# Kernel tuning notes

Hardware: AMD Instinct MI355X
Metric: run time of the kernel (lower is better)

## Reference

```python
import jax, jax.numpy as jnp
import numpy as np

DIM = 1024
HEADS = 16


def setup_inputs() -> dict:
    key = jax.random.key(0)
    ks = jax.random.split(key, 8)
    b, n, d = 2, 2048, DIM
    x = jax.random.normal(ks[0], (b, n, d), dtype=jnp.float32)
    # Linear(dim, 3*dim, bias=False): weight stored as [dim, 3*dim] (pre-transposed)
    W_qkv = jax.random.normal(ks[1], (d, 3 * d), dtype=jnp.float32) * (d ** -0.5)
    # Linear(dim, dim) with bias
    W_out = jax.random.normal(ks[2], (d, d), dtype=jnp.float32) * (d ** -0.5)
    b_out = jnp.zeros((d,), dtype=jnp.float32)
    alpha = jnp.ones((1,), dtype=jnp.float32)
    beta = jnp.zeros((1,), dtype=jnp.float32) + 0.5  # nonzero so softmax path is exercised
    gamma = jnp.zeros((1,), dtype=jnp.float32) + 0.1
    return {"x": x, "W_qkv": W_qkv, "W_out": W_out, "b_out": b_out,
            "alpha": alpha, "beta": beta, "gamma": gamma}


def reference(x, W_qkv, W_out, b_out, alpha, beta, gamma):
    b, n, d = x.shape
    h = HEADS
    hd = d // h
    scale = d ** -0.5  # note: full dim, as in the original module
    qkv = x @ W_qkv  # [b, n, 3d]
    q, k, v = jnp.split(qkv, 3, axis=-1)
    # [b, n, d] -> [b, h, n, hd]
    to_heads = lambda t: t.reshape(b, n, h, hd).transpose(0, 2, 1, 3)
    q, k, v = to_heads(q), to_heads(k), to_heads(v)
    dots = jnp.einsum("bhqd,bhkd->bhqk", q, k) * scale  # [b, h, n, n]
    attn = (alpha[0] * jnp.eye(n, dtype=x.dtype)
            + beta[0] * jax.nn.softmax(dots, axis=-1)
            - gamma[0] / n)
    out = jnp.einsum("bhqk,bhkd->bhqd", attn, v)  # [b, h, n, hd]
    out = out.transpose(0, 2, 1, 3).reshape(b, n, d)
    return out @ W_out + b_out
```

## Files before the change

### kernel.cpp

```cpp
#include <hip/hip_runtime.h>
#include <hip/hip_bf16.h>

#define DEVI __device__ __forceinline__

typedef __attribute__((ext_vector_type(8))) short bf16x8;
typedef __attribute__((ext_vector_type(4))) short bf16x4;
typedef __attribute__((ext_vector_type(4))) float f32x4;

DEVI unsigned short f2bf(float f) {
    unsigned u = __float_as_uint(f);
    u += 0x7FFF + ((u >> 16) & 1);
    return (unsigned short)(u >> 16);
}
DEVI float bf2f(unsigned short h) {
    return __uint_as_float(((unsigned)h) << 16);
}
DEVI f32x4 mfma16(bf16x8 a, bf16x8 b, f32x4 c) {
    return __builtin_amdgcn_mfma_f32_16x16x32_bf16(a, b, c, 0, 0, 0);
}
DEVI void gload_lds16(const void* g, void* l) {
    __builtin_amdgcn_global_load_lds(
        (const __attribute__((address_space(1))) unsigned int*)g,
        (__attribute__((address_space(3))) unsigned int*)l, 16, 0, 0);
}

DEVI void wt_body(const float* __restrict__ W, unsigned short* __restrict__ Wt,
                  int N, int n0, int k0, float sc, int tid,
                  unsigned short (*T)[72])
{
#pragma unroll
    for (int j = 0; j < 4; ++j) {
        int idx = tid + j * 256;
        int kk = idx >> 4, c4 = (idx & 15) << 2;
        float4 v = *(const float4*)(W + (size_t)(k0 + kk) * N + n0 + c4);
        T[c4 + 0][kk] = f2bf(v.x * sc); T[c4 + 1][kk] = f2bf(v.y * sc);
        T[c4 + 2][kk] = f2bf(v.z * sc); T[c4 + 3][kk] = f2bf(v.w * sc);
    }
    __syncthreads();
#pragma unroll
    for (int j = 0; j < 4; ++j) {
        int idx = tid + j * 256;
        int n = idx >> 4, c4 = (idx & 15) << 2;
        *(bf16x4*)(Wt + (size_t)(n0 + n) * 1024 + k0 + c4) = *(bf16x4*)&T[n][c4];
    }
}

__global__ __launch_bounds__(256) void k_prep(
    const float* __restrict__ X, const float* __restrict__ Wqkv,
    const float* __restrict__ Wout,
    unsigned short* __restrict__ Xb, unsigned short* __restrict__ Wt1,
    unsigned short* __restrict__ Wt2)
{
    __shared__ unsigned short T[64][72];
    const int tid = threadIdx.x;
    const int bid = blockIdx.x;
    const float QSC = 1.4426950408889634f / 32.0f;
    if (bid < 1024) {
        int i = bid * 256 + tid;
#pragma unroll
        for (int j = 0; j < 4; ++j) {
            int idx = i + j * 262144;
            float4 v = *(const float4*)(X + (size_t)idx * 4);
            bf16x4 hv;
            hv[0] = (short)f2bf(v.x); hv[1] = (short)f2bf(v.y);
            hv[2] = (short)f2bf(v.z); hv[3] = (short)f2bf(v.w);
            *(bf16x4*)(Xb + (size_t)idx * 4) = hv;
        }
    } else if (bid < 1792) {
        int idx = bid - 1024;
        int n0 = (idx % 48) * 64, k0 = (idx / 48) * 64;
        wt_body(Wqkv, Wt1, 3072, n0, k0, (n0 < 1024) ? QSC : 1.0f, tid, T);
    } else {
        int idx = bid - 1792;
        int n0 = (idx & 15) * 64, k0 = (idx >> 4) * 64;
        wt_body(Wout, Wt2, 1024, n0, k0, 1.0f, tid, T);
    }
}

__global__ __launch_bounds__(256) void k_gemm1(
    const unsigned short* __restrict__ A, const unsigned short* __restrict__ B,
    unsigned short* __restrict__ C)
{
    __shared__ unsigned short Sh[18432];
    unsigned short* As = Sh;
    unsigned short* Bs = Sh + 8192;
    const int tid = threadIdx.x, lane = tid & 63, wid = tid >> 6;
    const int wr = (wid >> 1) * 64, wc = (wid & 1) * 64;
    const int row0 = blockIdx.y * 128, col0 = blockIdx.x * 128;
    const int rsel = lane & 15, kgr = (lane >> 4) * 8;
    const int lr = lane >> 3, lc = (lane & 7) * 8;

    f32x4 acc[4][4];
#pragma unroll
    for (int i = 0; i < 4; ++i)
#pragma unroll
        for (int j = 0; j < 4; ++j) acc[i][j] = (f32x4){0.f, 0.f, 0.f, 0.f};

    for (int k0 = 0; k0 < 1024; k0 += 64) {
        __syncthreads();
#pragma unroll
        for (int i = 0; i < 4; ++i) {
            int rb = wid * 32 + i * 8;
            gload_lds16(A + (size_t)(row0 + rb + lr) * 1024 + k0 + lc, As + rb * 64);
            gload_lds16(B + (size_t)(col0 + rb + lr) * 1024 + k0 + lc, Bs + rb * 64);
        }
        __syncthreads();
#pragma unroll
        for (int ks = 0; ks < 2; ++ks) {
            bf16x8 a[4], b[4];
            int ko = ks * 32 + kgr;
#pragma unroll
            for (int mi = 0; mi < 4; ++mi)
                a[mi] = *(const bf16x8*)(As + (wr + mi * 16 + rsel) * 64 + ko);
#pragma unroll
            for (int nj = 0; nj < 4; ++nj)
                b[nj] = *(const bf16x8*)(Bs + (wc + nj * 16 + rsel) * 64 + ko);
#pragma unroll
            for (int mi = 0; mi < 4; ++mi)
#pragma unroll
                for (int nj = 0; nj < 4; ++nj)
                    acc[mi][nj] = mfma16(a[mi], b[nj], acc[mi][nj]);
        }
    }
    __syncthreads();
    unsigned short (*wb)[72] = (unsigned short (*)[72])(Sh + wid * 4608);
    const int g4 = (lane >> 4) << 2;
#pragma unroll
    for (int mi = 0; mi < 4; ++mi)
#pragma unroll
        for (int nj = 0; nj < 4; ++nj)
#pragma unroll
            for (int r = 0; r < 4; ++r)
                wb[mi * 16 + g4 + r][nj * 16 + rsel] = f2bf(acc[mi][nj][r]);
#pragma unroll
    for (int rr = 0; rr < 8; ++rr) {
        int row = rr * 8 + (lane >> 3);
        int c8 = (lane & 7) * 8;
        bf16x8 v = *(const bf16x8*)&wb[row][c8];
        *(bf16x8*)(C + (size_t)(row0 + wr + row) * 3072 + col0 + wc + c8) = v;
    }
}

__global__ __launch_bounds__(256) void k_vt(
    const unsigned short* __restrict__ qkv, unsigned short* __restrict__ Vt,
    float* __restrict__ vsum)
{
    __shared__ unsigned short T[64][72];
    __shared__ float ps[64];
    const int tid = threadIdx.x, lane = tid & 63, wid = tid >> 6;
    const int bh = blockIdx.y, b = bh >> 4, h = bh & 15;
    const int n0 = blockIdx.x * 64;
    const unsigned short* src = qkv + (size_t)(b * 2048 + n0) * 3072 + 2048 + h * 64;
#pragma unroll
    for (int j = 0; j < 2; ++j) {
        int idx = tid + j * 256;
        int n = idx >> 3, c8 = (idx & 7) << 3;
        *(bf16x8*)&T[n][c8] = *(const bf16x8*)(src + (size_t)n * 3072 + c8);
    }
    if (tid < 64) ps[tid] = 0.f;
    __syncthreads();
#pragma unroll
    for (int i = 0; i < 16; ++i) {
        int dv = wid * 16 + i;
        Vt[((size_t)bh * 64 + dv) * 2048 + n0 + lane] = T[lane][dv];
    }
    {
        const int col = tid & 63, qtr = tid >> 6;
        float s = 0.f;
#pragma unroll
        for (int i = 0; i < 16; ++i) s += bf2f(T[qtr * 16 + i][col]);
        atomicAdd(&ps[col], s);
        __syncthreads();
        if (tid < 64) atomicAdd(&vsum[bh * 64 + tid], ps[tid]);
    }
}

__global__ __launch_bounds__(256) void k_attn(
    const unsigned short* __restrict__ qkv, const unsigned short* __restrict__ Vt,
    const float* __restrict__ vsum,
    const float* __restrict__ alpha_p, const float* __restrict__ beta_p,
    const float* __restrict__ gamma_p,
    unsigned short* __restrict__ AO)
{
    __shared__ unsigned short Ks[4][64][64];
    __shared__ unsigned short Vs[4][64][64];
    __shared__ unsigned short Ps[4][32][64];
    const int tid = threadIdx.x, lane = tid & 63, wid = tid >> 6;
    const int swz = (blockIdx.x & 7) * 64 + (blockIdx.x >> 3);
    const int bh = swz >> 4, qtb = swz & 15;
    const int b = bh >> 4, h = bh & 15;
    const int q0 = qtb * 128;
    const int rsel = lane & 15, g = lane >> 4;
    const int g4 = g << 2;
    const int wq0 = wid * 32;
    const int r7 = rsel & 7;

    bf16x8 bq[2][2];
#pragma unroll
    for (int qt = 0; qt < 2; ++qt) {
        const unsigned short* qrow =
            qkv + (size_t)(b * 2048 + q0 + wq0 + qt * 16 + rsel) * 3072 + h * 64;
        bq[qt][0] = *(const bf16x8*)(qrow + g * 8);
        bq[qt][1] = *(const bf16x8*)(qrow + 32 + g * 8);
    }

    const int sr = lane >> 3;
    const int ss = (lane & 7) ^ sr;
    const int rb0 = wid * 16, rb1 = wid * 16 + 8;
    const unsigned short* kp0 = qkv + (size_t)(b * 2048) * 3072 + 1024 + h * 64
                              + (size_t)(rb0 + sr) * 3072 + ss * 8;
    const unsigned short* kp1 = kp0 + (size_t)8 * 3072;
    const unsigned short* vp0 = Vt + (size_t)bh * 64 * 2048
                              + (size_t)(rb0 + sr) * 2048 + ss * 8;
    const unsigned short* vp1 = vp0 + (size_t)8 * 2048;
    const size_t KADV = (size_t)64 * 3072;

    f32x4 o[2][4], ol[2];
#pragma unroll
    for (int qt = 0; qt < 2; ++qt) {
#pragma unroll
        for (int dj = 0; dj < 4; ++dj) o[qt][dj] = (f32x4){0.f, 0.f, 0.f, 0.f};
        ol[qt] = (f32x4){0.f, 0.f, 0.f, 0.f};
    }
    bf16x8 ones;
#pragma unroll
    for (int e = 0; e < 8; ++e) ones[e] = (short)0x3F80;

#define STAGE(BUF)                                                             \
    {                                                                          \
        gload_lds16(kp0, &Ks[BUF][rb0][0]);                                    \
        gload_lds16(kp1, &Ks[BUF][rb1][0]);                                    \
        gload_lds16(vp0, &Vs[BUF][rb0][0]);                                    \
        gload_lds16(vp1, &Vs[BUF][rb1][0]);                                    \
        kp0 += KADV; kp1 += KADV; vp0 += 64; vp1 += 64;                        \
    }

    STAGE(0); STAGE(1);
    asm volatile("s_waitcnt vmcnt(0)" ::: "memory");
    __syncthreads();

#define QK(CUR, S)                                                             \
    {                                                                          \
        _Pragma("unroll")                                                      \
        for (int qt = 0; qt < 2; ++qt)                                         \
            _Pragma("unroll")                                                  \
            for (int kj = 0; kj < 4; ++kj)                                     \
                S[qt][kj] = (f32x4){0.f, 0.f, 0.f, 0.f};                       \
        __builtin_amdgcn_s_setprio(1);                                         \
        _Pragma("unroll")                                                      \
        for (int ks = 0; ks < 2; ++ks) {                                       \
            const int sl = ((ks * 4 + g) ^ r7) * 8;                            \
            bf16x8 ak[4];                                                      \
            _Pragma("unroll")                                                  \
            for (int kj = 0; kj < 4; ++kj)                                     \
                ak[kj] = *(const bf16x8*)(&Ks[CUR][kj * 16 + rsel][sl]);       \
            _Pragma("unroll")                                                  \
            for (int qt = 0; qt < 2; ++qt)                                     \
                _Pragma("unroll")                                              \
                for (int kj = 0; kj < 4; ++kj)                                 \
                    S[qt][kj] = mfma16(ak[kj], bq[qt][ks], S[qt][kj]);         \
        }                                                                      \
        __builtin_amdgcn_s_setprio(0);                                         \
    }

#define EPV(CUR, S)                                                            \
    {                                                                          \
        _Pragma("unroll")                                                      \
        for (int qt = 0; qt < 2; ++qt)                                         \
            _Pragma("unroll")                                                  \
            for (int kj = 0; kj < 4; ++kj) {                                   \
                float p0 = __builtin_amdgcn_exp2f(S[qt][kj][0]);               \
                float p1 = __builtin_amdgcn_exp2f(S[qt][kj][1]);               \
                float p2 = __builtin_amdgcn_exp2f(S[qt][kj][2]);               \
                float p3 = __builtin_amdgcn_exp2f(S[qt][kj][3]);               \
                union { __hip_bfloat162 h2[2]; uint2 u; } pk;                  \
                pk.h2[0] = __float22bfloat162_rn(make_float2(p0, p1));         \
                pk.h2[1] = __float22bfloat162_rn(make_float2(p2, p3));         \
                const int slot16 = (kj * 2 + (g >> 1)) ^ r7;                   \
                *(uint2*)(&Ps[wid][qt * 16 + rsel][slot16 * 8 + (g & 1) * 4])  \
                    = pk.u;                                                    \
            }                                                                  \
        __builtin_amdgcn_s_setprio(1);                                         \
        _Pragma("unroll")                                                      \
        for (int ks = 0; ks < 2; ++ks) {                                       \
            const int sl = ((ks * 4 + g) ^ r7) * 8;                            \
            bf16x8 pa0 = *(const bf16x8*)(&Ps[wid][rsel][sl]);                 \
            bf16x8 pa1 = *(const bf16x8*)(&Ps[wid][16 + rsel][sl]);            \
            bf16x8 vb[4];                                                      \
            _Pragma("unroll")                                                  \
            for (int dj = 0; dj < 4; ++dj)                                     \
                vb[dj] = *(const bf16x8*)(&Vs[CUR][dj * 16 + rsel][sl]);       \
            _Pragma("unroll")                                                  \
            for (int dj = 0; dj < 4; ++dj) {                                   \
                o[0][dj] = mfma16(pa0, vb[dj], o[0][dj]);                      \
                o[1][dj] = mfma16(pa1, vb[dj], o[1][dj]);                      \
            }                                                                  \
            ol[0] = mfma16(pa0, ones, ol[0]);                                  \
            ol[1] = mfma16(pa1, ones, ol[1]);                                  \
        }                                                                      \
        __builtin_amdgcn_s_setprio(0);                                         \
    }

#define PAIR(C0, C1, DOPF)                                                     \
    {                                                                          \
        f32x4 s0[2][4], s1[2][4];                                              \
        if (DOPF) { STAGE(C0 ^ 2); STAGE(C1 ^ 2); }                            \
        QK(C0, s0);                                                            \
        QK(C1, s1);                                                            \
        EPV(C0, s0);                                                           \
        EPV(C1, s1);                                                           \
        asm volatile("s_waitcnt vmcnt(0)" ::: "memory");                       \
        __syncthreads();                                                       \
    }

#pragma unroll 1
    for (int i = 0; i < 8; ++i) {
        PAIR(0, 1, true);
        PAIR(2, 3, (i < 7));
    }
#undef PAIR
#undef EPV
#undef QK
#undef STAGE

    const float alpha = *alpha_p, beta = *beta_p;
    const float gn = (*gamma_p) / 2048.0f;
#pragma unroll
    for (int qt = 0; qt < 2; ++qt) {
        float linv[4];
#pragma unroll
        for (int r = 0; r < 4; ++r)
            linv[r] = beta / ol[qt][r];
#pragma unroll
        for (int dj = 0; dj < 4; ++dj)
#pragma unroll
            for (int r = 0; r < 4; ++r) {
                int qrow = q0 + wq0 + qt * 16 + g4 + r;
                int dv = dj * 16 + rsel;
                float ov = o[qt][dj][r] * linv[r];
                float vdiag = bf2f(qkv[(size_t)(b * 2048 + qrow) * 3072 + 2048 + h * 64 + dv]);
                float vs = vsum[bh * 64 + dv];
                float res = ov + alpha * vdiag - gn * vs;
                AO[(size_t)(b * 2048 + qrow) * 1024 + h * 64 + dv] = f2bf(res);
            }
    }
}

__global__ __launch_bounds__(256) void k_gemm2(
    const unsigned short* __restrict__ A, const unsigned short* __restrict__ B,
    const float* __restrict__ bias, float* __restrict__ Out)
{
    __shared__ unsigned short As[64 * 64];
    __shared__ unsigned short Bs[64 * 64];
    const int tid = threadIdx.x, lane = tid & 63, wid = tid >> 6;
    const int wr = (wid >> 1) * 32, wc = (wid & 1) * 32;
    const int row0 = blockIdx.y * 64, col0 = blockIdx.x * 64;
    const int rsel = lane & 15, kgr = (lane >> 4) * 8;
    const int lr = lane >> 3, lc = (lane & 7) * 8;

    f32x4 acc[2][2];
#pragma unroll
    for (int i = 0; i < 2; ++i)
#pragma unroll
        for (int j = 0; j < 2; ++j) acc[i][j] = (f32x4){0.f, 0.f, 0.f, 0.f};

    for (int k0 = 0; k0 < 1024; k0 += 64) {
        __syncthreads();
#pragma unroll
        for (int i = 0; i < 2; ++i) {
            int rb = wid * 16 + i * 8;
            gload_lds16(A + (size_t)(row0 + rb + lr) * 1024 + k0 + lc, As + rb * 64);
            gload_lds16(B + (size_t)(col0 + rb + lr) * 1024 + k0 + lc, Bs + rb * 64);
        }
        __syncthreads();
#pragma unroll
        for (int ks = 0; ks < 2; ++ks) {
            bf16x8 a[2], b[2];
            int ko = ks * 32 + kgr;
#pragma unroll
            for (int mi = 0; mi < 2; ++mi)
                a[mi] = *(const bf16x8*)(As + (wr + mi * 16 + rsel) * 64 + ko);
#pragma unroll
            for (int nj = 0; nj < 2; ++nj)
                b[nj] = *(const bf16x8*)(Bs + (wc + nj * 16 + rsel) * 64 + ko);
#pragma unroll
            for (int mi = 0; mi < 2; ++mi)
#pragma unroll
                for (int nj = 0; nj < 2; ++nj)
                    acc[mi][nj] = mfma16(a[mi], b[nj], acc[mi][nj]);
        }
    }
    const int rbase = row0 + wr + ((lane >> 4) << 2);
    const int cbase = col0 + wc + rsel;
#pragma unroll
    for (int mi = 0; mi < 2; ++mi)
#pragma unroll
        for (int nj = 0; nj < 2; ++nj) {
            int gc = cbase + nj * 16;
            float bv = bias[gc];
#pragma unroll
            for (int r = 0; r < 4; ++r)
                Out[(size_t)(rbase + mi * 16 + r) * 1024 + gc] = acc[mi][nj][r] + bv;
        }
}

extern "C" void kernel_launch(void* const* d_in, const int* in_sizes, int n_in,
                              void* d_out, int out_size, void* d_ws, size_t ws_size,
                              hipStream_t stream) {
    const float* x     = (const float*)d_in[0];
    const float* Wqkv  = (const float*)d_in[1];
    const float* Wout  = (const float*)d_in[2];
    const float* bout  = (const float*)d_in[3];
    const float* alpha = (const float*)d_in[4];
    const float* beta  = (const float*)d_in[5];
    const float* gamma = (const float*)d_in[6];
    float* out = (float*)d_out;

    char* ws = (char*)d_ws;
    unsigned short* Xb  = (unsigned short*)(ws);
    unsigned short* Wt1 = (unsigned short*)(ws + 8388608);
    unsigned short* Wt2 = (unsigned short*)(ws + 14680064);
    unsigned short* qkv = (unsigned short*)(ws + 16777216);
    unsigned short* Vt  = (unsigned short*)(ws + 41943040);
    float* vsum         = (float*)(ws + 50331648);
    unsigned short* AO  = Xb;

    hipMemsetAsync(vsum, 0, 2048 * sizeof(float), stream);
    k_prep<<<2048, 256, 0, stream>>>(x, Wqkv, Wout, Xb, Wt1, Wt2);
    k_gemm1<<<dim3(24, 32), 256, 0, stream>>>(Xb, Wt1, qkv);
    k_vt<<<dim3(32, 32), 256, 0, stream>>>(qkv, Vt, vsum);
    k_attn<<<512, 256, 0, stream>>>(qkv, Vt, vsum, alpha, beta, gamma, AO);
    k_gemm2<<<dim3(16, 64), 256, 0, stream>>>(AO, Wt2, bout, out);
}
```

Measured before the change: 141.2 us.

## Fuse V transpose and column-sum into GEMM1 epilogue, fold memset into prep

Removes the separate k_vt kernel. The QKV GEMM epilogue now writes the transposed V tile from its LDS staging buffer and accumulates per-head V column sums with shuffles and atomics. The vsum memset is moved into block 0 of the prep kernel. This saves two launches and a re-read of V from global memory. In exchange, the V-column GEMM blocks do extra scattered 2-byte stores and more atomics. The sums now come from fp32 accumulators rather than bf16-rounded values.

```diff
diff --git a/kernel.cpp b/kernel.cpp
--- a/kernel.cpp
+++ b/kernel.cpp
@@ -49,13 +49,18 @@
     const float* __restrict__ X, const float* __restrict__ Wqkv,
     const float* __restrict__ Wout,
     unsigned short* __restrict__ Xb, unsigned short* __restrict__ Wt1,
-    unsigned short* __restrict__ Wt2)
+    unsigned short* __restrict__ Wt2, float* __restrict__ vsum)
 {
     __shared__ unsigned short T[64][72];
     const int tid = threadIdx.x;
     const int bid = blockIdx.x;
     const float QSC = 1.4426950408889634f / 32.0f;
     if (bid < 1024) {
+        if (bid == 0) {
+            float4 z = (float4){0.f, 0.f, 0.f, 0.f};
+            ((float4*)vsum)[tid] = z;
+            ((float4*)vsum)[tid + 256] = z;
+        }
         int i = bid * 256 + tid;
 #pragma unroll
         for (int j = 0; j < 4; ++j) {
@@ -79,7 +84,8 @@
 
 __global__ __launch_bounds__(256) void k_gemm1(
     const unsigned short* __restrict__ A, const unsigned short* __restrict__ B,
-    unsigned short* __restrict__ C)
+    unsigned short* __restrict__ C, unsigned short* __restrict__ Vt,
+    float* __restrict__ vsum)
 {
     __shared__ unsigned short Sh[18432];
     unsigned short* As = Sh;
@@ -139,39 +145,26 @@
         bf16x8 v = *(const bf16x8*)&wb[row][c8];
         *(bf16x8*)(C + (size_t)(row0 + wr + row) * 3072 + col0 + wc + c8) = v;
     }
-}
-
-__global__ __launch_bounds__(256) void k_vt(
-    const unsigned short* __restrict__ qkv, unsigned short* __restrict__ Vt,
-    float* __restrict__ vsum)
-{
-    __shared__ unsigned short T[64][72];
-    __shared__ float ps[64];
-    const int tid = threadIdx.x, lane = tid & 63, wid = tid >> 6;
-    const int bh = blockIdx.y, b = bh >> 4, h = bh & 15;
-    const int n0 = blockIdx.x * 64;
-    const unsigned short* src = qkv + (size_t)(b * 2048 + n0) * 3072 + 2048 + h * 64;
-#pragma unroll
-    for (int j = 0; j < 2; ++j) {
-        int idx = tid + j * 256;
-        int n = idx >> 3, c8 = (idx & 7) << 3;
-        *(bf16x8*)&T[n][c8] = *(const bf16x8*)(src + (size_t)n * 3072 + c8);
-    }
-    if (tid < 64) ps[tid] = 0.f;
-    __syncthreads();
-#pragma unroll
-    for (int i = 0; i < 16; ++i) {
-        int dv = wid * 16 + i;
-        Vt[((size_t)bh * 64 + dv) * 2048 + n0 + lane] = T[lane][dv];
-    }
-    {
-        const int col = tid & 63, qtr = tid >> 6;
-        float s = 0.f;
-#pragma unroll
-        for (int i = 0; i < 16; ++i) s += bf2f(T[qtr * 16 + i][col]);
-        atomicAdd(&ps[col], s);
-        __syncthreads();
-        if (tid < 64) atomicAdd(&vsum[bh * 64 + tid], ps[tid]);
+
+    if (col0 >= 2048) {
+        const int b_ = row0 >> 11;
+        const int n0 = (row0 & 2047) + wr;
+        const int bh = b_ * 16 + ((col0 + wc - 2048) >> 6);
+#pragma unroll
+        for (int nj = 0; nj < 4; ++nj) {
+            float s = 0.f;
+#pragma unroll
+            for (int mi = 0; mi < 4; ++mi)
+#pragma unroll
+                for (int r = 0; r < 4; ++r) s += acc[mi][nj][r];
+            s += __shfl_xor(s, 16);
+            s += __shfl_xor(s, 32);
+            if (lane < 16) atomicAdd(&vsum[bh * 64 + nj * 16 + rsel], s);
+        }
+        unsigned short* vtb = Vt + (size_t)bh * 64 * 2048 + n0 + lane;
+#pragma unroll 8
+        for (int dv = 0; dv < 64; ++dv)
+            vtb[(size_t)dv * 2048] = wb[lane][dv];
     }
 }
 
@@ -425,10 +418,8 @@
     float* vsum         = (float*)(ws + 50331648);
     unsigned short* AO  = Xb;
 
-    hipMemsetAsync(vsum, 0, 2048 * sizeof(float), stream);
-    k_prep<<<2048, 256, 0, stream>>>(x, Wqkv, Wout, Xb, Wt1, Wt2);
-    k_gemm1<<<dim3(24, 32), 256, 0, stream>>>(Xb, Wt1, qkv);
-    k_vt<<<dim3(32, 32), 256, 0, stream>>>(qkv, Vt, vsum);
+    k_prep<<<2048, 256, 0, stream>>>(x, Wqkv, Wout, Xb, Wt1, Wt2, vsum);
+    k_gemm1<<<dim3(24, 32), 256, 0, stream>>>(Xb, Wt1, qkv, Vt, vsum);
     k_attn<<<512, 256, 0, stream>>>(qkv, Vt, vsum, alpha, beta, gamma, AO);
     k_gemm2<<<dim3(16, 64), 256, 0, stream>>>(AO, Wt2, bout, out);
 }
```

New measurement: 132.8 us. 5.9% less time.
